# Kernel optimization log

Measured on AMD Instinct MI355X. Metric: run time of the kernel, lower is better.

The kernel has to match this reference:

```python
import jax, jax.numpy as jnp
import numpy as np

B, N, INDIM, OUTDIM = 32, 128, 32, 64


def setup_inputs() -> dict:
    key = jax.random.key(0)
    k1, k2, k3, k4, k5, k6 = jax.random.split(key, 6)
    X = jax.random.normal(k1, (B, N, N, INDIM), dtype=jnp.float32)
    # variable subgraph sizes (irregular masking), at least 1 node per graph
    n_nodes = jnp.clip(jax.random.randint(k2, (B,), 0, N), 1, N).astype(jnp.int64)
    # MLP params (Linear + ReLU tail activation) for lin1 and lin2
    s = 1.0 / np.sqrt(INDIM)
    W1 = jax.random.uniform(k3, (INDIM, OUTDIM), jnp.float32, -s, s)
    b1 = jax.random.uniform(k4, (OUTDIM,), jnp.float32, -s, s)
    W2 = jax.random.uniform(k5, (INDIM, OUTDIM), jnp.float32, -s, s)
    b2 = jax.random.uniform(k6, (OUTDIM,), jnp.float32, -s, s)
    return {"X": X, "W1": W1, "b1": b1, "W2": W2, "b2": b2, "n_nodes": n_nodes}


def reference(X, W1, b1, W2, b2, n_nodes):
    # pairwise mask [B,N,N,1] from per-graph node counts (MaskedTensor mode 'DD')
    nm = jnp.arange(N)[None, :] < n_nodes[:, None]          # [B,N] node mask
    mask = (nm[:, :, None] & nm[:, None, :])[..., None].astype(X.dtype)  # [B,N,N,1]
    # tuplewiseapply of lin1 / lin2 (Linear + ReLU), zero-fill masked tuples
    X1 = jax.nn.relu(jnp.einsum('bijd,de->bije', X, W1) + b1) * mask  # [B,N,N,OUTDIM]
    X2 = jax.nn.relu(jnp.einsum('bijd,de->bije', X, W2) + b2) * mask
    # Op2FWL (aggr='sum'): per-channel batched matmul over node dim k
    out = jnp.einsum('bike,bkje->bije', X1, X2) * mask
    return out
```

## Files before the change

kernel.cpp:

```cpp
#include <hip/hip_runtime.h>

typedef unsigned short ushort_t;
typedef __attribute__((ext_vector_type(8))) __bf16 bf16x8;
typedef __attribute__((ext_vector_type(4))) float f32x4;


__device__ __forceinline__ ushort_t f32_to_bf16(float v) {
    unsigned ui = __float_as_uint(v);
    ui += 0x7fffu + ((ui >> 16) & 1u);
    return (ushort_t)(ui >> 16);
}

union FragU { bf16x8 f; ushort_t u[8]; };
union Pack4 { ushort_t us[4]; uint2 v; };

__global__ __launch_bounds__(256) void lin_mfma_kernel(
        const float* __restrict__ X,
        const float* __restrict__ W1, const float* __restrict__ b1v,
        const float* __restrict__ W2, const float* __restrict__ b2v,
        const int* __restrict__ n_nodes,
        ushort_t* __restrict__ X1t, ushort_t* __restrict__ X2t) {
    __shared__ ushort_t sO[64 * 136];
    const int blk = blockIdx.x;
    const int pass = blk >> 10;
    const int idx = blk & 1023;
    const int b = idx >> 5, rg = idx & 31;
    const float* W    = pass ? W2  : W1;
    const float* bias = pass ? b2v : b1v;
    ushort_t* Out     = pass ? X2t : X1t;
    const int rstride = pass ? 32 : 4096;
    const int tstride = pass ? 4096 : 32;

    const int u = threadIdx.x;
    const int w = u >> 6, l = u & 63;
    const int quad = l >> 4, lid = l & 15;
    const int n = n_nodes[b];

    FragU bfrag[4];
    float bia[4];
    #pragma unroll
    for (int ni = 0; ni < 4; ++ni) {
        const int e = ni * 16 + lid;
        #pragma unroll
        for (int j = 0; j < 8; ++j)
            bfrag[ni].u[j] = f32_to_bf16(W[(quad * 8 + j) * 64 + e]);
        bia[ni] = bias[e];
    }

    for (int q = 0; q < 4; ++q) {
        const int r = rg * 4 + q;
        const bool rin = (r < n);
        if (rin) {
            const float* Xb = X + (size_t)b * 524288 + (size_t)r * rstride;
            #pragma unroll
            for (int s = 0; s < 2; ++s) {
                const int mt = w * 2 + s;
                const int t0b = mt * 16 + quad * 4;
                if (mt * 16 < n) {
                    const int m = mt * 16 + lid;
                    const float* xr = Xb + (size_t)m * tstride + quad * 8;
                    float4 x0 = *(const float4*)xr;
                    float4 x1 = *(const float4*)(xr + 4);
                    FragU af;
                    af.u[0] = f32_to_bf16(x0.x); af.u[1] = f32_to_bf16(x0.y);
                    af.u[2] = f32_to_bf16(x0.z); af.u[3] = f32_to_bf16(x0.w);
                    af.u[4] = f32_to_bf16(x1.x); af.u[5] = f32_to_bf16(x1.y);
                    af.u[6] = f32_to_bf16(x1.z); af.u[7] = f32_to_bf16(x1.w);
                    #pragma unroll
                    for (int ni = 0; ni < 4; ++ni) {
                        f32x4 acc = {};
                        acc = __builtin_amdgcn_mfma_f32_16x16x32_bf16(
                            af.f, bfrag[ni].f, acc, 0, 0, 0);
                        const int e = ni * 16 + lid;
                        Pack4 pk;
                        #pragma unroll
                        for (int rgi = 0; rgi < 4; ++rgi) {
                            const int t = t0b + rgi;
                            float v = (t < n) ? fmaxf(acc[rgi] + bia[ni], 0.f) : 0.f;
                            pk.us[rgi] = f32_to_bf16(v);
                        }
                        *(uint2*)(sO + e * 136 + t0b) = pk.v;
                    }
                } else {
                    Pack4 pk; pk.us[0] = pk.us[1] = pk.us[2] = pk.us[3] = 0;
                    #pragma unroll
                    for (int ni = 0; ni < 4; ++ni)
                        *(uint2*)(sO + (ni * 16 + lid) * 136 + t0b) = pk.v;
                }
            }
        }
        __syncthreads();
        {
            const int e = u >> 2, part = u & 3;
            ushort_t* gO = Out + ((size_t)(b * 64 + e) * 128 + r) * 128 + part * 32;
            if (rin) {
                const ushort_t* sRow = sO + e * 136 + part * 32;
                #pragma unroll
                for (int c = 0; c < 4; ++c)
                    *(uint4*)(gO + c * 8) = *(const uint4*)(sRow + c * 8);
            } else {
                uint4 z = {0, 0, 0, 0};
                #pragma unroll
                for (int c = 0; c < 4; ++c)
                    *(uint4*)(gO + c * 8) = z;
            }
        }
        __syncthreads();
    }
}

__global__ __launch_bounds__(256) void mm_kernel(
        const ushort_t* __restrict__ X1t, const ushort_t* __restrict__ X2t,
        ushort_t* __restrict__ Ct, const int* __restrict__ n_nodes) {
    __shared__ ushort_t sC[128 * 136];
    const int blk = blockIdx.x;
    const size_t plane = (size_t)blk * 16384;
    const int n = n_nodes[blk >> 6];
    const int kmax = (n + 31) & ~31;
    const ushort_t* Aj = X2t + plane;
    const ushort_t* Bi = X1t + plane;
    const int u = threadIdx.x;
    const int w = u >> 6, l = u & 63;
    const int quad = l >> 4, lid = l & 15;
    const int wj = (w >> 1) * 64, wi = (w & 1) * 64;
    const bool anyA = (wj < n), anyB = (wi < n);
    bool aAct[4], bAct[4];
    #pragma unroll
    for (int mj = 0; mj < 4; ++mj) aAct[mj] = (wj + mj * 16) < n;
    #pragma unroll
    for (int ni = 0; ni < 4; ++ni) bAct[ni] = (wi + ni * 16) < n;
    f32x4 acc[4][4] = {};

    for (int k0 = 0; k0 < kmax; k0 += 32) {
        bf16x8 af[4], bfr[4];
        #pragma unroll
        for (int mj = 0; mj < 4; ++mj)
            if (aAct[mj] && anyB)
                af[mj] = *(const bf16x8*)(Aj + (size_t)(wj + mj * 16 + lid) * 128 + k0 + quad * 8);
        #pragma unroll
        for (int ni = 0; ni < 4; ++ni)
            if (bAct[ni] && anyA)
                bfr[ni] = *(const bf16x8*)(Bi + (size_t)(wi + ni * 16 + lid) * 128 + k0 + quad * 8);
        #pragma unroll
        for (int mj = 0; mj < 4; ++mj)
            #pragma unroll
            for (int ni = 0; ni < 4; ++ni)
                if (aAct[mj] && bAct[ni])
                    acc[mj][ni] = __builtin_amdgcn_mfma_f32_16x16x32_bf16(
                        af[mj], bfr[ni], acc[mj][ni], 0, 0, 0);
    }

    #pragma unroll
    for (int mj = 0; mj < 4; ++mj)
        #pragma unroll
        for (int ni = 0; ni < 4; ++ni) {
            const int j0 = wj + mj * 16 + quad * 4;
            const int i  = wi + ni * 16 + lid;
            Pack4 pk;
            #pragma unroll
            for (int rg = 0; rg < 4; ++rg)
                pk.us[rg] = f32_to_bf16(acc[mj][ni][rg]);
            *(uint2*)(sC + i * 136 + j0) = pk.v;
        }
    __syncthreads();
    ushort_t* Cp = Ct + plane;
    #pragma unroll
    for (int it = 0; it < 8; ++it) {
        int idx = it * 256 + u;
        int i = idx >> 4, c = idx & 15;
        *(uint4*)(Cp + (size_t)idx * 8) = *(const uint4*)(sC + i * 136 + c * 8);
    }
}

__global__ __launch_bounds__(256) void tr_kernel(
        const ushort_t* __restrict__ Ct, float* __restrict__ out,
        const int* __restrict__ n_nodes) {
    __shared__ float sT[64 * 129];
    const int blk = blockIdx.x;
    const int b = blk >> 7, i = blk & 127;
    const int u = threadIdx.x;
    const int n = n_nodes[b];
    float* ob = out + ((size_t)b * 16384 + (size_t)i * 128) * 64;

    if (i >= n) {
        float4 z = {0.f, 0.f, 0.f, 0.f};
        #pragma unroll
        for (int it = 0; it < 8; ++it)
            *(float4*)(ob + (size_t)(it * 256 + u) * 4) = z;
        return;
    }

    const ushort_t* Cb = Ct + (size_t)b * 1048576 + (size_t)i * 128;
    #pragma unroll
    for (int it = 0; it < 4; ++it) {
        int idx = it * 256 + u;
        int e = idx >> 4, c = idx & 15;
        float* dst = sT + e * 129 + c * 8;
        if (c * 8 < n) {
            uint4 v = *(const uint4*)(Cb + (size_t)e * 16384 + c * 8);
            dst[0] = __uint_as_float(v.x << 16);
            dst[1] = __uint_as_float(v.x & 0xffff0000u);
            dst[2] = __uint_as_float(v.y << 16);
            dst[3] = __uint_as_float(v.y & 0xffff0000u);
            dst[4] = __uint_as_float(v.z << 16);
            dst[5] = __uint_as_float(v.z & 0xffff0000u);
            dst[6] = __uint_as_float(v.w << 16);
            dst[7] = __uint_as_float(v.w & 0xffff0000u);
        } else {
            #pragma unroll
            for (int t = 0; t < 8; ++t) dst[t] = 0.f;
        }
    }
    __syncthreads();

    #pragma unroll
    for (int it = 0; it < 8; ++it) {
        int idx = it * 256 + u;
        int j = idx >> 4, e0 = (idx & 15) * 4;
        float4 vv;
        vv.x = sT[(e0 + 0) * 129 + j];
        vv.y = sT[(e0 + 1) * 129 + j];
        vv.z = sT[(e0 + 2) * 129 + j];
        vv.w = sT[(e0 + 3) * 129 + j];
        *(float4*)(ob + (size_t)idx * 4) = vv;
    }
}

extern "C" void kernel_launch(void* const* d_in, const int* in_sizes, int n_in,
                              void* d_out, int out_size, void* d_ws, size_t ws_size,
                              hipStream_t stream) {
    const float* X  = (const float*)d_in[0];
    const float* W1 = (const float*)d_in[1];
    const float* b1 = (const float*)d_in[2];
    const float* W2 = (const float*)d_in[3];
    const float* b2 = (const float*)d_in[4];
    const int* nn   = (const int*)d_in[5];
    float* out = (float*)d_out;

    ushort_t* X1t = (ushort_t*)d_ws;
    ushort_t* X2t = X1t + 33554432;
    ushort_t* Ct  = X1t;

    lin_mfma_kernel<<<2048, 256, 0, stream>>>(X, W1, b1, W2, b2, nn, X1t, X2t);
    mm_kernel<<<2048, 256, 0, stream>>>(X1t, X2t, Ct, nn);
    tr_kernel<<<4096, 256, 0, stream>>>(Ct, out, nn);
}
```

Before: 270.5 us.

## Fuse per-channel matmul and transpose into one tiled output kernel

Replaces the separate per-channel bf16 matmul kernel and the transpose/convert kernel with one kernel. Each block computes a 16x16 (i,j) tile across all 64 channels and writes fp32 output directly in [b,i,j,e] layout through shared memory. This removes the bf16 intermediate C round-trip through global memory and one kernel launch. In exchange each wave runs a serial chain of single MFMAs with no operand reuse across tiles, so each X1/X2 row is reloaded by 8 blocks and operand loads go up. The bf16 rounding of the intermediate result is also removed.

```diff
diff --git a/kernel.cpp b/kernel.cpp
--- a/kernel.cpp
+++ b/kernel.cpp
@@ -109,120 +109,62 @@
     }
 }
 
-__global__ __launch_bounds__(256) void mm_kernel(
+__global__ __launch_bounds__(256) void mmtr_kernel(
         const ushort_t* __restrict__ X1t, const ushort_t* __restrict__ X2t,
-        ushort_t* __restrict__ Ct, const int* __restrict__ n_nodes) {
-    __shared__ ushort_t sC[128 * 136];
+        float* __restrict__ out, const int* __restrict__ n_nodes) {
+    __shared__ float sOut[16640];
     const int blk = blockIdx.x;
-    const size_t plane = (size_t)blk * 16384;
-    const int n = n_nodes[blk >> 6];
-    const int kmax = (n + 31) & ~31;
-    const ushort_t* Aj = X2t + plane;
-    const ushort_t* Bi = X1t + plane;
+    const int b = blk >> 6, it = (blk >> 3) & 7, jt = blk & 7;
+    const int n = n_nodes[b];
+    const int i0 = it * 16, j0 = jt * 16;
     const int u = threadIdx.x;
-    const int w = u >> 6, l = u & 63;
-    const int quad = l >> 4, lid = l & 15;
-    const int wj = (w >> 1) * 64, wi = (w & 1) * 64;
-    const bool anyA = (wj < n), anyB = (wi < n);
-    bool aAct[4], bAct[4];
-    #pragma unroll
-    for (int mj = 0; mj < 4; ++mj) aAct[mj] = (wj + mj * 16) < n;
-    #pragma unroll
-    for (int ni = 0; ni < 4; ++ni) bAct[ni] = (wi + ni * 16) < n;
-    f32x4 acc[4][4] = {};
+    float* ob = out + (size_t)b * 1048576 + (size_t)i0 * 8192 + (size_t)j0 * 64;
 
-    for (int k0 = 0; k0 < kmax; k0 += 32) {
-        bf16x8 af[4], bfr[4];
-        #pragma unroll
-        for (int mj = 0; mj < 4; ++mj)
-            if (aAct[mj] && anyB)
-                af[mj] = *(const bf16x8*)(Aj + (size_t)(wj + mj * 16 + lid) * 128 + k0 + quad * 8);
-        #pragma unroll
-        for (int ni = 0; ni < 4; ++ni)
-            if (bAct[ni] && anyA)
-                bfr[ni] = *(const bf16x8*)(Bi + (size_t)(wi + ni * 16 + lid) * 128 + k0 + quad * 8);
-        #pragma unroll
-        for (int mj = 0; mj < 4; ++mj)
-            #pragma unroll
-            for (int ni = 0; ni < 4; ++ni)
-                if (aAct[mj] && bAct[ni])
-                    acc[mj][ni] = __builtin_amdgcn_mfma_f32_16x16x32_bf16(
-                        af[mj], bfr[ni], acc[mj][ni], 0, 0, 0);
-    }
-
-    #pragma unroll
-    for (int mj = 0; mj < 4; ++mj)
-        #pragma unroll
-        for (int ni = 0; ni < 4; ++ni) {
-            const int j0 = wj + mj * 16 + quad * 4;
-            const int i  = wi + ni * 16 + lid;
-            Pack4 pk;
-            #pragma unroll
-            for (int rg = 0; rg < 4; ++rg)
-                pk.us[rg] = f32_to_bf16(acc[mj][ni][rg]);
-            *(uint2*)(sC + i * 136 + j0) = pk.v;
-        }
-    __syncthreads();
-    ushort_t* Cp = Ct + plane;
-    #pragma unroll
-    for (int it = 0; it < 8; ++it) {
-        int idx = it * 256 + u;
-        int i = idx >> 4, c = idx & 15;
-        *(uint4*)(Cp + (size_t)idx * 8) = *(const uint4*)(sC + i * 136 + c * 8);
-    }
-}
-
-__global__ __launch_bounds__(256) void tr_kernel(
-        const ushort_t* __restrict__ Ct, float* __restrict__ out,
-        const int* __restrict__ n_nodes) {
-    __shared__ float sT[64 * 129];
-    const int blk = blockIdx.x;
-    const int b = blk >> 7, i = blk & 127;
-    const int u = threadIdx.x;
-    const int n = n_nodes[b];
-    float* ob = out + ((size_t)b * 16384 + (size_t)i * 128) * 64;
-
-    if (i >= n) {
+    if (i0 >= n || j0 >= n) {
         float4 z = {0.f, 0.f, 0.f, 0.f};
         #pragma unroll
-        for (int it = 0; it < 8; ++it)
-            *(float4*)(ob + (size_t)(it * 256 + u) * 4) = z;
+        for (int itx = 0; itx < 16; ++itx) {
+            int idx = itx * 256 + u;
+            int i = idx >> 8, rem = idx & 255;
+            int j = rem >> 4, e4 = (rem & 15) * 4;
+            *(float4*)(ob + (size_t)i * 8192 + j * 64 + e4) = z;
+        }
         return;
     }
 
-    const ushort_t* Cb = Ct + (size_t)b * 1048576 + (size_t)i * 128;
-    #pragma unroll
-    for (int it = 0; it < 4; ++it) {
-        int idx = it * 256 + u;
-        int e = idx >> 4, c = idx & 15;
-        float* dst = sT + e * 129 + c * 8;
-        if (c * 8 < n) {
-            uint4 v = *(const uint4*)(Cb + (size_t)e * 16384 + c * 8);
-            dst[0] = __uint_as_float(v.x << 16);
-            dst[1] = __uint_as_float(v.x & 0xffff0000u);
-            dst[2] = __uint_as_float(v.y << 16);
-            dst[3] = __uint_as_float(v.y & 0xffff0000u);
-            dst[4] = __uint_as_float(v.z << 16);
-            dst[5] = __uint_as_float(v.z & 0xffff0000u);
-            dst[6] = __uint_as_float(v.w << 16);
-            dst[7] = __uint_as_float(v.w & 0xffff0000u);
-        } else {
-            #pragma unroll
-            for (int t = 0; t < 8; ++t) dst[t] = 0.f;
+    const int kmax = (n + 31) & ~31;
+    const int w = u >> 6, l = u & 63;
+    const int quad = l >> 4, lid = l & 15;
+    const ushort_t* Ab = X1t + (size_t)b * 1048576 + (size_t)(i0 + lid) * 128;
+    const ushort_t* Bb = X2t + (size_t)b * 1048576 + (size_t)(j0 + lid) * 128;
+
+    for (int t = 0; t < 16; ++t) {
+        const int e = w * 16 + t;
+        const ushort_t* Ae = Ab + (size_t)e * 16384;
+        const ushort_t* Be = Bb + (size_t)e * 16384;
+        f32x4 acc = {};
+        for (int k0 = 0; k0 < kmax; k0 += 32) {
+            bf16x8 af = *(const bf16x8*)(Ae + k0 + quad * 8);
+            bf16x8 bf = *(const bf16x8*)(Be + k0 + quad * 8);
+            acc = __builtin_amdgcn_mfma_f32_16x16x32_bf16(af, bf, acc, 0, 0, 0);
         }
+        float* so = sOut + (quad * 4) * 1040 + lid * 65 + e;
+        so[0]    = acc[0];
+        so[1040] = acc[1];
+        so[2080] = acc[2];
+        so[3120] = acc[3];
     }
     __syncthreads();
 
     #pragma unroll
-    for (int it = 0; it < 8; ++it) {
-        int idx = it * 256 + u;
-        int j = idx >> 4, e0 = (idx & 15) * 4;
-        float4 vv;
-        vv.x = sT[(e0 + 0) * 129 + j];
-        vv.y = sT[(e0 + 1) * 129 + j];
-        vv.z = sT[(e0 + 2) * 129 + j];
-        vv.w = sT[(e0 + 3) * 129 + j];
-        *(float4*)(ob + (size_t)idx * 4) = vv;
+    for (int itx = 0; itx < 16; ++itx) {
+        int idx = itx * 256 + u;
+        int i = idx >> 8, rem = idx & 255;
+        int j = rem >> 4, e4 = (rem & 15) * 4;
+        const float* sp = sOut + i * 1040 + j * 65 + e4;
+        float4 v;
+        v.x = sp[0]; v.y = sp[1]; v.z = sp[2]; v.w = sp[3];
+        *(float4*)(ob + (size_t)i * 8192 + j * 64 + e4) = v;
     }
 }
 
@@ -239,9 +181,7 @@
 
     ushort_t* X1t = (ushort_t*)d_ws;
     ushort_t* X2t = X1t + 33554432;
-    ushort_t* Ct  = X1t;
 
     lin_mfma_kernel<<<2048, 256, 0, stream>>>(X, W1, b1, W2, b2, nn, X1t, X2t);
-    mm_kernel<<<2048, 256, 0, stream>>>(X1t, X2t, Ct, nn);
-    tr_kernel<<<4096, 256, 0, stream>>>(Ct, out, nn);
+    mmtr_kernel<<<2048, 256, 0, stream>>>(X1t, X2t, out, nn);
 }
```

Result: slower. 299.5 us (+10.7%).
